# Performance work log

Hardware: AMD Instinct MI355X
Metric: run time of the kernel (lower is better)

Reference implementation:

```python
import jax, jax.numpy as jnp
import numpy as np

POS_HALF = 4   # positive window: [t-4, t+4)
NEG_LEN = 12   # negatives: up to 12 frames on each side of the positive window
K_MAX = 2 * POS_HALF + 2 * NEG_LEN  # 32 candidates max per timestep


def _build_windows(T):
    """Static [T,K_MAX] gather indices + positive/valid masks (numpy, trace-time)."""
    idx = np.zeros((T, K_MAX), np.int32)
    pos_mask = np.zeros((T, K_MAX), bool)
    valid = np.zeros((T, K_MAX), bool)
    for t in range(T):
        start, end = max(0, t - POS_HALF), min(T, t + POS_HALF)
        pos = list(range(start, end))
        neg = list(range(max(0, start - NEG_LEN), start)) + \
              list(range(end, min(T, end + NEG_LEN)))
        comb = pos + neg
        idx[t, :len(comb)] = comb
        valid[t, :len(comb)] = True
        pos_mask[t, :len(pos)] = True
    return jnp.asarray(idx), jnp.asarray(pos_mask), jnp.asarray(valid)


def _directional(q, kv, idx, pos_mask, valid, scale, bias):
    # q, kv: [B,T,D] (L2-normalized); idx/pos_mask/valid: [T,K]
    w = kv[:, idx]  # [B,T,K,D] windowed gather
    logits = jnp.einsum('btd,btkd->btk', q, w) * scale + bias  # [B,T,K]
    sign = jnp.where(pos_mask, 1.0, -1.0)
    loglik = jax.nn.log_sigmoid(sign * logits)
    # per-t: sum over window, mean over batch; then sum over t
    loss = -jnp.where(valid, loglik, 0.0).sum(axis=2).mean(axis=0).sum()
    am = jnp.argmax(jnp.where(valid, logits, -jnp.inf), axis=2)  # [B,T]
    T = q.shape[1]
    correct = pos_mask[jnp.arange(T)[None, :], am].astype(jnp.float32).sum()
    return loss, correct


def setup_inputs() -> dict:
    key = jax.random.key(0)
    k1, k2 = jax.random.split(key)
    B, T, D = 8, 1024, 512
    return {
        "motion_feature": jax.random.normal(k1, (B, T, D), jnp.float32),
        "audio_feature": jax.random.normal(k2, (B, T, D), jnp.float32),
        "logit_scale": jnp.asarray(np.log(1.0 / 0.07), jnp.float32),  # param (pre-exp)
        "logit_bias": jnp.asarray(0.0, jnp.float32),                  # param
    }


def reference(motion_feature, audio_feature, logit_scale, logit_bias):
    B, T, _ = motion_feature.shape
    eps = 1e-12
    m = motion_feature / jnp.clip(
        jnp.linalg.norm(motion_feature, axis=2, keepdims=True), eps)
    a = audio_feature / jnp.clip(
        jnp.linalg.norm(audio_feature, axis=2, keepdims=True), eps)
    scale = jnp.exp(logit_scale)
    idx, pos_mask, valid = _build_windows(T)
    m2a_loss, m2a_correct = _directional(m, a, idx, pos_mask, valid, scale, logit_bias)
    a2m_loss, a2m_correct = _directional(a, m, idx, pos_mask, valid, scale, logit_bias)
    final_loss = (m2a_loss + a2m_loss) / (2 * T)
    total_correct = (m2a_correct + a2m_correct) / (2 * T * B)
    return final_loss, total_correct
```

## Files before the change

kernel.cpp:

```cpp
#include <hip/hip_runtime.h>
#include <hip/hip_bf16.h>
#include <math.h>

#define B_DIM 8
#define T_DIM 1024
#define D_DIM 512
#define BT (B_DIM * T_DIM)
#define NBLK 512

typedef __bf16 bf16x8 __attribute__((ext_vector_type(8)));
typedef float floatx4 __attribute__((ext_vector_type(4)));

__device__ __forceinline__ float wave_reduce_sum(float v) {
#pragma unroll
    for (int off = 32; off > 0; off >>= 1) v += __shfl_xor(v, off, 64);
    return v;
}

__device__ __forceinline__ float softplus(float y) {
    return fmaxf(y, 0.0f) + __logf(1.0f + __expf(-fabsf(y)));
}

__device__ __forceinline__ bf16x8 cvt8(float4 x, float4 y) {
    union { ushort u[8]; bf16x8 v; } r;
    __hip_bfloat162 h0 = __float22bfloat162_rn(make_float2(x.x, x.y));
    __hip_bfloat162 h1 = __float22bfloat162_rn(make_float2(x.z, x.w));
    __hip_bfloat162 h2 = __float22bfloat162_rn(make_float2(y.x, y.y));
    __hip_bfloat162 h3 = __float22bfloat162_rn(make_float2(y.z, y.w));
    ushort2 p0 = *(ushort2*)&h0, p1 = *(ushort2*)&h1;
    ushort2 p2 = *(ushort2*)&h2, p3 = *(ushort2*)&h3;
    r.u[0] = p0.x; r.u[1] = p0.y; r.u[2] = p1.x; r.u[3] = p1.y;
    r.u[4] = p2.x; r.u[5] = p2.y; r.u[6] = p3.x; r.u[7] = p3.y;
    return r.v;
}

__global__ __launch_bounds__(512, 4) void crossband_kernel(
    const float* __restrict__ m, const float* __restrict__ a,
    const float* __restrict__ pscale, const float* __restrict__ pbias,
    float* __restrict__ part_loss, float* __restrict__ part_corr)
{
    __shared__ float red[8][5][272];
    __shared__ float Sbuf[48][49];
    __shared__ float red2[8][6][16];
    __shared__ float norms[6][16];
    __shared__ float rowpos[16], colpos[16], shl[8];

    int blk = blockIdx.x;
    int b   = blk & 7;
    int t0  = (blk >> 3) << 4;
    int tid  = threadIdx.x;
    int w    = tid >> 6;
    int lane = tid & 63;
    int mrow = lane & 15;
    int kgrp = lane >> 4;
    int koff = w * 64 + kgrp * 8;

    const float* mb = m + ((size_t)b << 19);
    const float* ab = a + ((size_t)b << 19);

    const float* mp[3]; const float* ap[3];
#pragma unroll
    for (int s = 0; s < 3; ++s) {
        int r = t0 - 16 + s * 16 + mrow;
        r = min(max(r, 0), T_DIM - 1);
        mp[s] = mb + (size_t)r * D_DIM + koff;
        ap[s] = ab + (size_t)r * D_DIM + koff;
    }

    floatx4 acc[5];
#pragma unroll
    for (int q = 0; q < 5; ++q) acc[q] = (floatx4){0.f,0.f,0.f,0.f};
    float ssm[3] = {0.f,0.f,0.f}, ssa[3] = {0.f,0.f,0.f};

#pragma unroll
    for (int ks = 0; ks < 2; ++ks) {
        bf16x8 am[3], av[3];
#pragma unroll
        for (int s = 0; s < 3; ++s) {
            float4 x = *(const float4*)(mp[s] + ks * 32);
            float4 y = *(const float4*)(mp[s] + ks * 32 + 4);
            ssm[s] += x.x*x.x + x.y*x.y + x.z*x.z + x.w*x.w
                    + y.x*y.x + y.y*y.y + y.z*y.z + y.w*y.w;
            am[s] = cvt8(x, y);
            float4 u = *(const float4*)(ap[s] + ks * 32);
            float4 v = *(const float4*)(ap[s] + ks * 32 + 4);
            ssa[s] += u.x*u.x + u.y*u.y + u.z*u.z + u.w*u.w
                    + v.x*v.x + v.y*v.y + v.z*v.z + v.w*v.w;
            av[s] = cvt8(u, v);
        }
        acc[0] = __builtin_amdgcn_mfma_f32_16x16x32_bf16(am[1], av[0], acc[0], 0, 0, 0);
        acc[1] = __builtin_amdgcn_mfma_f32_16x16x32_bf16(am[1], av[1], acc[1], 0, 0, 0);
        acc[2] = __builtin_amdgcn_mfma_f32_16x16x32_bf16(am[1], av[2], acc[2], 0, 0, 0);
        acc[3] = __builtin_amdgcn_mfma_f32_16x16x32_bf16(am[0], av[1], acc[3], 0, 0, 0);
        acc[4] = __builtin_amdgcn_mfma_f32_16x16x32_bf16(am[2], av[1], acc[4], 0, 0, 0);
    }

#pragma unroll
    for (int off = 16; off <= 32; off <<= 1) {
#pragma unroll
        for (int s = 0; s < 3; ++s) {
            ssm[s] += __shfl_xor(ssm[s], off, 64);
            ssa[s] += __shfl_xor(ssa[s], off, 64);
        }
    }
    if (kgrp == 0) {
#pragma unroll
        for (int s = 0; s < 3; ++s) {
            red2[w][s][mrow]     = ssm[s];
            red2[w][3 + s][mrow] = ssa[s];
        }
    }
#pragma unroll
    for (int q = 0; q < 5; ++q)
#pragma unroll
        for (int r = 0; r < 4; ++r)
            red[w][q][(kgrp * 4 + r) * 17 + mrow] = acc[q][r];
    __syncthreads();

    if (tid < 96) {
        int slot = tid >> 4, mr = tid & 15;
        float ss = 0.f;
#pragma unroll
        for (int ww = 0; ww < 8; ++ww) ss += red2[ww][slot][mr];
        norms[slot][mr] = 1.0f / fmaxf(sqrtf(ss), 1e-12f);
    }
    {
        const int tu[5] = {16, 16, 16, 0, 32};
        const int tv[5] = {0, 16, 32, 16, 16};
#pragma unroll
        for (int e = 0; e < 3; ++e) {
            int idx = tid + e * 512;
            if (idx < 1280) {
                int q = idx >> 8, r2 = idx & 255;
                int rho = r2 >> 4, kap = r2 & 15;
                float s4 = 0.f;
#pragma unroll
                for (int ww = 0; ww < 8; ++ww)
                    s4 += red[ww][q][rho * 17 + kap];
                Sbuf[tu[q] + rho][tv[q] + kap] = s4;
            }
        }
    }
    __syncthreads();

    float scale = expf(pscale[0]), bias = pbias[0];
    float loss = 0.0f;

    if (tid < 256) {
        int i = tid >> 4, cc = tid & 15;
        float im_u = norms[1][i];
        float mmax = -1e30f, mpos = 0.0f;
#pragma unroll
        for (int tj = 0; tj < 3; ++tj) {
            int v  = tj * 16 + cc;
            int dd = v - i;
            int c  = t0 - 16 + v;
            if (dd >= 0 && dd < 32 && c >= 0 && c < T_DIM) {
                float sv = Sbuf[16 + i][v] * norms[3 + tj][cc];
                float logit = sv * im_u * scale + bias;
                bool pos = (dd >= 12) && (dd <= 19);
                loss += softplus(pos ? -logit : logit);
                if (sv > mmax) { mmax = sv; mpos = pos ? 1.0f : 0.0f; }
            }
        }
#pragma unroll
        for (int off = 1; off < 16; off <<= 1) {
            float ov = __shfl_xor(mmax, off, 64);
            float op = __shfl_xor(mpos, off, 64);
            if (ov > mmax) { mmax = ov; mpos = op; }
        }
        if (cc == 0) rowpos[i] = mpos;
    } else {
        int t2 = tid - 256;
        int i = t2 >> 4, cc = t2 & 15;
        float ia_v = norms[4][i];
        float amax = -1e30f, apos = 0.0f;
#pragma unroll
        for (int tj = 0; tj < 3; ++tj) {
            int u2 = tj * 16 + cc;
            int ee = u2 - i;
            int r  = t0 - 16 + u2;
            if (ee >= 0 && ee < 32 && r >= 0 && r < T_DIM) {
                float sv = Sbuf[u2][16 + i] * norms[tj][cc];
                float logit = sv * ia_v * scale + bias;
                bool pos = (ee >= 12) && (ee <= 19);
                loss += softplus(pos ? -logit : logit);
                if (sv > amax) { amax = sv; apos = pos ? 1.0f : 0.0f; }
            }
        }
#pragma unroll
        for (int off = 1; off < 16; off <<= 1) {
            float ov = __shfl_xor(amax, off, 64);
            float op = __shfl_xor(apos, off, 64);
            if (ov > amax) { amax = ov; apos = op; }
        }
        if (cc == 0) colpos[i] = apos;
    }

    loss = wave_reduce_sum(loss);
    if (lane == 0) shl[w] = loss;
    __syncthreads();
    if (tid == 0) {
        float L = 0.0f, C = 0.0f;
#pragma unroll
        for (int r = 0; r < 8; ++r) L += shl[r];
#pragma unroll
        for (int r = 0; r < 16; ++r) C += rowpos[r] + colpos[r];
        part_loss[blk] = L;
        part_corr[blk] = C;
    }
}

__global__ __launch_bounds__(256) void finalsum_kernel(
    const float* __restrict__ part_loss, const float* __restrict__ part_corr,
    float* __restrict__ out)
{
    int tid = threadIdx.x;
    float l = part_loss[tid] + part_loss[tid + 256];
    float c = part_corr[tid] + part_corr[tid + 256];
    l = wave_reduce_sum(l);
    c = wave_reduce_sum(c);
    __shared__ float shl[4], shc[4];
    int w = tid >> 6, lane = tid & 63;
    if (lane == 0) { shl[w] = l; shc[w] = c; }
    __syncthreads();
    if (tid == 0) {
        out[0] = (shl[0] + shl[1] + shl[2] + shl[3]) / 16384.0f;
        out[1] = (shc[0] + shc[1] + shc[2] + shc[3]) / 16384.0f;
    }
}

extern "C" void kernel_launch(void* const* d_in, const int* in_sizes, int n_in,
                              void* d_out, int out_size, void* d_ws, size_t ws_size,
                              hipStream_t stream)
{
    const float* m  = (const float*)d_in[0];
    const float* a  = (const float*)d_in[1];
    const float* ps = (const float*)d_in[2];
    const float* pb = (const float*)d_in[3];
    float* out = (float*)d_out;

    float* part_loss = (float*)d_ws;
    float* part_corr = part_loss + NBLK;

    crossband_kernel<<<NBLK, 512, 0, stream>>>(m, a, ps, pb,
                                               part_loss, part_corr);
    finalsum_kernel<<<1, 256, 0, stream>>>(part_loss, part_corr, out);
}
```

Measured before the change: 90.90 us.

## Enlarge block tile to 32 timesteps with bf16 LDS staging and full-K MFMA tiles

Each block now covers 32 timesteps (64 halo rows) instead of 16 (48 rows), which cuts redundant global reads of neighbouring rows. Rows are converted to bf16 and staged in shared memory. Each of 8 waves then computes one 16x16 band tile over the full K dimension, which removes the per-wave K-split and the cross-wave LDS reduction. The cost is large LDS use per block, which limits occupancy, and half as many blocks.

```diff
diff --git a/kernel.cpp b/kernel.cpp
--- a/kernel.cpp
+++ b/kernel.cpp
@@ -5,8 +5,7 @@
 #define B_DIM 8
 #define T_DIM 1024
 #define D_DIM 512
-#define BT (B_DIM * T_DIM)
-#define NBLK 512
+#define NBLK 256
 
 typedef __bf16 bf16x8 __attribute__((ext_vector_type(8)));
 typedef float floatx4 __attribute__((ext_vector_type(4)));
@@ -34,130 +33,91 @@
     return r.v;
 }
 
-__global__ __launch_bounds__(512, 4) void crossband_kernel(
+__global__ __launch_bounds__(1024, 4) void crossband_kernel(
     const float* __restrict__ m, const float* __restrict__ a,
     const float* __restrict__ pscale, const float* __restrict__ pbias,
     float* __restrict__ part_loss, float* __restrict__ part_corr)
 {
-    __shared__ float red[8][5][272];
-    __shared__ float Sbuf[48][49];
-    __shared__ float red2[8][6][16];
-    __shared__ float norms[6][16];
-    __shared__ float rowpos[16], colpos[16], shl[8];
-
-    int blk = blockIdx.x;
-    int b   = blk & 7;
-    int t0  = (blk >> 3) << 4;
-    int tid  = threadIdx.x;
-    int w    = tid >> 6;
-    int lane = tid & 63;
-    int mrow = lane & 15;
-    int kgrp = lane >> 4;
-    int koff = w * 64 + kgrp * 8;
-
-    const float* mb = m + ((size_t)b << 19);
-    const float* ab = a + ((size_t)b << 19);
-
-    const float* mp[3]; const float* ap[3];
-#pragma unroll
-    for (int s = 0; s < 3; ++s) {
-        int r = t0 - 16 + s * 16 + mrow;
-        r = min(max(r, 0), T_DIM - 1);
-        mp[s] = mb + (size_t)r * D_DIM + koff;
-        ap[s] = ab + (size_t)r * D_DIM + koff;
-    }
-
-    floatx4 acc[5];
-#pragma unroll
-    for (int q = 0; q < 5; ++q) acc[q] = (floatx4){0.f,0.f,0.f,0.f};
-    float ssm[3] = {0.f,0.f,0.f}, ssa[3] = {0.f,0.f,0.f};
-
-#pragma unroll
-    for (int ks = 0; ks < 2; ++ks) {
-        bf16x8 am[3], av[3];
-#pragma unroll
-        for (int s = 0; s < 3; ++s) {
-            float4 x = *(const float4*)(mp[s] + ks * 32);
-            float4 y = *(const float4*)(mp[s] + ks * 32 + 4);
-            ssm[s] += x.x*x.x + x.y*x.y + x.z*x.z + x.w*x.w
-                    + y.x*y.x + y.y*y.y + y.z*y.z + y.w*y.w;
-            am[s] = cvt8(x, y);
-            float4 u = *(const float4*)(ap[s] + ks * 32);
-            float4 v = *(const float4*)(ap[s] + ks * 32 + 4);
-            ssa[s] += u.x*u.x + u.y*u.y + u.z*u.z + u.w*u.w
-                    + v.x*v.x + v.y*v.y + v.z*v.z + v.w*v.w;
-            av[s] = cvt8(u, v);
-        }
-        acc[0] = __builtin_amdgcn_mfma_f32_16x16x32_bf16(am[1], av[0], acc[0], 0, 0, 0);
-        acc[1] = __builtin_amdgcn_mfma_f32_16x16x32_bf16(am[1], av[1], acc[1], 0, 0, 0);
-        acc[2] = __builtin_amdgcn_mfma_f32_16x16x32_bf16(am[1], av[2], acc[2], 0, 0, 0);
-        acc[3] = __builtin_amdgcn_mfma_f32_16x16x32_bf16(am[0], av[1], acc[3], 0, 0, 0);
-        acc[4] = __builtin_amdgcn_mfma_f32_16x16x32_bf16(am[2], av[1], acc[4], 0, 0, 0);
-    }
-
-#pragma unroll
-    for (int off = 16; off <= 32; off <<= 1) {
-#pragma unroll
-        for (int s = 0; s < 3; ++s) {
-            ssm[s] += __shfl_xor(ssm[s], off, 64);
-            ssa[s] += __shfl_xor(ssa[s], off, 64);
-        }
-    }
-    if (kgrp == 0) {
-#pragma unroll
-        for (int s = 0; s < 3; ++s) {
-            red2[w][s][mrow]     = ssm[s];
-            red2[w][3 + s][mrow] = ssa[s];
-        }
-    }
-#pragma unroll
-    for (int q = 0; q < 5; ++q)
-#pragma unroll
-        for (int r = 0; r < 4; ++r)
-            red[w][q][(kgrp * 4 + r) * 17 + mrow] = acc[q][r];
-    __syncthreads();
-
-    if (tid < 96) {
-        int slot = tid >> 4, mr = tid & 15;
-        float ss = 0.f;
-#pragma unroll
-        for (int ww = 0; ww < 8; ++ww) ss += red2[ww][slot][mr];
-        norms[slot][mr] = 1.0f / fmaxf(sqrtf(ss), 1e-12f);
-    }
+    __shared__ __align__(16) ushort Abf[64][520];
+    __shared__ __align__(16) ushort Bbf[64][520];
+    __shared__ float Sbuf[64][65];
+    __shared__ float normM[64], normA[64];
+    __shared__ float rowpos[32], colpos[32], shl[16];
+
+    const int blk = blockIdx.x;
+    const int b   = blk & 7;
+    const int t0  = (blk >> 3) << 5;
+    const int tid  = threadIdx.x;
+    const int w    = tid >> 6;
+    const int lane = tid & 63;
+
     {
-        const int tu[5] = {16, 16, 16, 0, 32};
-        const int tv[5] = {0, 16, 32, 16, 16};
-#pragma unroll
-        for (int e = 0; e < 3; ++e) {
-            int idx = tid + e * 512;
-            if (idx < 1280) {
-                int q = idx >> 8, r2 = idx & 255;
-                int rho = r2 >> 4, kap = r2 & 15;
-                float s4 = 0.f;
-#pragma unroll
-                for (int ww = 0; ww < 8; ++ww)
-                    s4 += red[ww][q][rho * 17 + kap];
-                Sbuf[tu[q] + rho][tv[q] + kap] = s4;
-            }
-        }
-    }
-    __syncthreads();
-
-    float scale = expf(pscale[0]), bias = pbias[0];
+        const int j = tid >> 4, p = tid & 15;
+        const int r = min(max(t0 - 16 + j, 0), T_DIM - 1);
+        const float* mr = m + ((size_t)b << 19) + (size_t)r * D_DIM + p * 32;
+        const float* ar = a + ((size_t)b << 19) + (size_t)r * D_DIM + p * 32;
+        float ssm = 0.f, ssa = 0.f;
+#pragma unroll
+        for (int c = 0; c < 4; ++c) {
+            float4 x = *(const float4*)(mr + c * 8);
+            float4 y = *(const float4*)(mr + c * 8 + 4);
+            ssm += x.x*x.x + x.y*x.y + x.z*x.z + x.w*x.w
+                 + y.x*y.x + y.y*y.y + y.z*y.z + y.w*y.w;
+            *(bf16x8*)&Abf[j][p * 32 + c * 8] = cvt8(x, y);
+            float4 u = *(const float4*)(ar + c * 8);
+            float4 v = *(const float4*)(ar + c * 8 + 4);
+            ssa += u.x*u.x + u.y*u.y + u.z*u.z + u.w*u.w
+                 + v.x*v.x + v.y*v.y + v.z*v.z + v.w*v.w;
+            *(bf16x8*)&Bbf[j][p * 32 + c * 8] = cvt8(u, v);
+        }
+#pragma unroll
+        for (int off = 1; off <= 8; off <<= 1) {
+            ssm += __shfl_xor(ssm, off, 64);
+            ssa += __shfl_xor(ssa, off, 64);
+        }
+        if (p == 0) {
+            normM[j] = 1.0f / fmaxf(sqrtf(ssm), 1e-12f);
+            normA[j] = 1.0f / fmaxf(sqrtf(ssa), 1e-12f);
+        }
+    }
+    __syncthreads();
+
+    if (w < 8) {
+        const int rt = (0xCA95 >> (2 * w)) & 3;
+        const int ct = (0x9E64 >> (2 * w)) & 3;
+        const int mrow = lane & 15, kgrp = lane >> 4;
+        floatx4 acc = (floatx4){0.f, 0.f, 0.f, 0.f};
+        const ushort* arow = &Abf[rt * 16 + mrow][kgrp * 8];
+        const ushort* brow = &Bbf[ct * 16 + mrow][kgrp * 8];
+#pragma unroll
+        for (int c = 0; c < 16; ++c) {
+            bf16x8 af  = *(const bf16x8*)(arow + c * 32);
+            bf16x8 bfr = *(const bf16x8*)(brow + c * 32);
+            acc = __builtin_amdgcn_mfma_f32_16x16x32_bf16(af, bfr, acc, 0, 0, 0);
+        }
+#pragma unroll
+        for (int q = 0; q < 4; ++q)
+            Sbuf[rt * 16 + kgrp * 4 + q][ct * 16 + mrow] = acc[q];
+    }
+    __syncthreads();
+
+    const float scale = expf(pscale[0]);
+    const float bias  = pbias[0];
     float loss = 0.0f;
 
-    if (tid < 256) {
-        int i = tid >> 4, cc = tid & 15;
-        float im_u = norms[1][i];
+    if (tid < 512) {
+        int i2 = tid >> 4, cc = tid & 15;
+        int s2 = i2 >> 4;
+        float im = normM[16 + i2];
         float mmax = -1e30f, mpos = 0.0f;
 #pragma unroll
         for (int tj = 0; tj < 3; ++tj) {
-            int v  = tj * 16 + cc;
-            int dd = v - i;
+            int v  = (s2 + tj) * 16 + cc;
+            int dd = v - i2;
             int c  = t0 - 16 + v;
             if (dd >= 0 && dd < 32 && c >= 0 && c < T_DIM) {
-                float sv = Sbuf[16 + i][v] * norms[3 + tj][cc];
-                float logit = sv * im_u * scale + bias;
+                float sv = Sbuf[16 + i2][v] * normA[v];
+                float logit = sv * im * scale + bias;
                 bool pos = (dd >= 12) && (dd <= 19);
                 loss += softplus(pos ? -logit : logit);
                 if (sv > mmax) { mmax = sv; mpos = pos ? 1.0f : 0.0f; }
@@ -169,20 +129,21 @@
             float op = __shfl_xor(mpos, off, 64);
             if (ov > mmax) { mmax = ov; mpos = op; }
         }
-        if (cc == 0) rowpos[i] = mpos;
+        if (cc == 0) rowpos[i2] = mpos;
     } else {
-        int t2 = tid - 256;
-        int i = t2 >> 4, cc = t2 & 15;
-        float ia_v = norms[4][i];
+        int t2 = tid - 512;
+        int i2 = t2 >> 4, cc = t2 & 15;
+        int s2 = i2 >> 4;
+        float ia = normA[16 + i2];
         float amax = -1e30f, apos = 0.0f;
 #pragma unroll
         for (int tj = 0; tj < 3; ++tj) {
-            int u2 = tj * 16 + cc;
-            int ee = u2 - i;
-            int r  = t0 - 16 + u2;
-            if (ee >= 0 && ee < 32 && r >= 0 && r < T_DIM) {
-                float sv = Sbuf[u2][16 + i] * norms[tj][cc];
-                float logit = sv * ia_v * scale + bias;
+            int u2 = (s2 + tj) * 16 + cc;
+            int ee = u2 - i2;
+            int rr = t0 - 16 + u2;
+            if (ee >= 0 && ee < 32 && rr >= 0 && rr < T_DIM) {
+                float sv = Sbuf[u2][16 + i2] * normM[u2];
+                float logit = sv * ia * scale + bias;
                 bool pos = (ee >= 12) && (ee <= 19);
                 loss += softplus(pos ? -logit : logit);
                 if (sv > amax) { amax = sv; apos = pos ? 1.0f : 0.0f; }
@@ -194,7 +155,7 @@
             float op = __shfl_xor(apos, off, 64);
             if (ov > amax) { amax = ov; apos = op; }
         }
-        if (cc == 0) colpos[i] = apos;
+        if (cc == 0) colpos[i2] = apos;
     }
 
     loss = wave_reduce_sum(loss);
@@ -203,9 +164,9 @@
     if (tid == 0) {
         float L = 0.0f, C = 0.0f;
 #pragma unroll
-        for (int r = 0; r < 8; ++r) L += shl[r];
-#pragma unroll
-        for (int r = 0; r < 16; ++r) C += rowpos[r] + colpos[r];
+        for (int q = 0; q < 16; ++q) L += shl[q];
+#pragma unroll
+        for (int q = 0; q < 32; ++q) C += rowpos[q] + colpos[q];
         part_loss[blk] = L;
         part_corr[blk] = C;
     }
@@ -216,8 +177,8 @@
     float* __restrict__ out)
 {
     int tid = threadIdx.x;
-    float l = part_loss[tid] + part_loss[tid + 256];
-    float c = part_corr[tid] + part_corr[tid + 256];
+    float l = part_loss[tid];
+    float c = part_corr[tid];
     l = wave_reduce_sum(l);
     c = wave_reduce_sum(c);
     __shared__ float shl[4], shc[4];
@@ -243,7 +204,7 @@
     float* part_loss = (float*)d_ws;
     float* part_corr = part_loss + NBLK;
 
-    crossband_kernel<<<NBLK, 512, 0, stream>>>(m, a, ps, pb,
-                                               part_loss, part_corr);
+    crossband_kernel<<<NBLK, 1024, 0, stream>>>(m, a, ps, pb,
+                                                part_loss, part_corr);
     finalsum_kernel<<<1, 256, 0, stream>>>(part_loss, part_corr, out);
 }
```

Result: faster. 87.68 us (-3.5%).
